# Kernel optimization log

Hardware: AMD Instinct MI355X
Metric: run time of the kernel (lower is better)

The kernel has to match this reference:

```python
import jax, jax.numpy as jnp
import numpy as np

B, NPG, DEG = 256, 128, 16          # graphs per side, nodes per graph, avg degree
N = B * NPG                          # 32768 nodes per side
E = N * DEG                          # 524288 edges per side
F_IN, F1, F2, F3 = 64, 128, 64, 32   # number_labels, filters_1..3
TN, BINS = 16, 16                    # tensor_neurons, bins


def setup_inputs() -> dict:
    key = jax.random.key(0)
    ks = jax.random.split(key, 24)

    def make_edges(k):
        # random edges, each constrained within its own graph block
        base = jax.random.randint(k, (2, E), 0, NPG)
        off = jnp.repeat(jnp.arange(B, dtype=jnp.int64) * NPG, NPG * DEG)
        return (base + off[None, :]).astype(jnp.int64)

    def w(k, shape, fan_in):
        return (jax.random.normal(k, shape, jnp.float32) / np.sqrt(fan_in)).astype(jnp.float32)

    batch = jnp.repeat(jnp.arange(B, dtype=jnp.int64), NPG)
    return {
        'x1': jax.random.normal(ks[0], (N, F_IN), jnp.float32),
        'edge_index_1': make_edges(ks[1]),
        'batch_1': batch,
        'x2': jax.random.normal(ks[2], (N, F_IN), jnp.float32),
        'edge_index_2': make_edges(ks[3]),
        'batch_2': batch,
        # GCN layer params
        'W1': w(ks[4], (F_IN, F1), F_IN), 'b1': jnp.zeros((F1,), jnp.float32),
        'W2': w(ks[5], (F1, F2), F1),     'b2': jnp.zeros((F2,), jnp.float32),
        'W3': w(ks[6], (F2, F3), F2),     'b3': jnp.zeros((F3,), jnp.float32),
        # attention pooling
        'attW': w(ks[7], (F3, F3), F3),
        # tensor network module
        'tW': w(ks[8], (F3, F3, TN), F3),
        'tblock': w(ks[9], (TN, 2 * F3), 2 * F3),
        'tbias': jnp.zeros((TN,), jnp.float32),
        # scoring MLP (feature_count = TN + BINS -> 16 -> 1)
        'sW1': w(ks[10], (TN + BINS, 16), TN + BINS), 'sb1': jnp.zeros((16,), jnp.float32),
        'sW2': w(ks[11], (16, 1), 16),                'sb2': jnp.zeros((1,), jnp.float32),
    }


def _gcn(x, W, b, src, dst):
    # PyG GCNConv: add self-loops, symmetric deg^-1/2 normalization, then scatter-add
    n = x.shape[0]
    loop = jnp.arange(n, dtype=src.dtype)
    s = jnp.concatenate([src, loop])
    d = jnp.concatenate([dst, loop])
    deg = jax.ops.segment_sum(jnp.ones_like(d, dtype=x.dtype), d, num_segments=n)
    dinv = jax.lax.rsqrt(jnp.maximum(deg, 1e-12))
    norm = dinv[s] * dinv[d]                      # [E+N]
    h = x @ W                                     # [N, Fout]
    out = jax.ops.segment_sum(norm[:, None] * h[s], d, num_segments=n)
    return out + b


def _histc(v):
    # torch.histc with bins=BINS, min=max=0 -> uses data min/max; last bin inclusive
    v = v.reshape(-1)
    lo, hi = v.min(), v.max()
    idx = jnp.floor((v - lo) / jnp.maximum(hi - lo, 1e-12) * BINS)
    idx = jnp.clip(idx, 0, BINS - 1).astype(jnp.int32)
    h = jax.ops.segment_sum(jnp.ones_like(v), idx, num_segments=BINS)
    return h / h.sum()


def reference(x1, edge_index_1, batch_1, x2, edge_index_2, batch_2,
              W1, b1, W2, b2, W3, b3, attW, tW, tblock, tbias,
              sW1, sb1, sW2, sb2):
    def conv_pass(x, ei):
        src, dst = ei[0], ei[1]
        h = jax.nn.relu(_gcn(x, W1, b1, src, dst))   # dropout inactive (eval)
        h = jax.nn.relu(_gcn(h, W2, b2, src, dst))
        return _gcn(h, W3, b3, src, dst)

    f1 = conv_pass(x1, edge_index_1)
    f2 = conv_pass(x2, edge_index_2)

    # to_dense_batch: equal-sized, batch-sorted graphs -> plain reshape, full masks
    d1 = f1.reshape(B, NPG, F3)
    d2 = f2.reshape(B, NPG, F3)

    # per-graph-pair similarity histogram (detached in original)
    scores = jnp.einsum('bnd,bmd->bnm', jax.lax.stop_gradient(d1), jax.lax.stop_gradient(d2))
    hist = jax.vmap(_histc)(jax.nn.sigmoid(scores))  # [B, BINS]

    # attention pooling (SimGNN AttentionModule)
    def attn_pool(d):
        ctx = jnp.tanh(jnp.mean(d @ attW, axis=1))             # [B, F3]
        att = jax.nn.sigmoid(jnp.einsum('bnd,bd->bn', d, ctx))  # [B, NPG]
        return jnp.einsum('bnd,bn->bd', d, att)                 # [B, F3]

    e1 = attn_pool(d1)
    e2 = attn_pool(d2)

    # tensor network scoring
    tensor_scores = jnp.einsum('bi,ijk,bj->bk', e1, tW, e2)
    block_scores = jnp.concatenate([e1, e2], axis=-1) @ tblock.T
    tnm = jax.nn.relu(tensor_scores + block_scores + tbias)      # [B, TN]

    feat = jnp.concatenate([tnm, hist], axis=1)                  # [B, TN+BINS]
    h = jax.nn.relu(feat @ sW1 + sb1)
    score = jax.nn.sigmoid(h @ sW2 + sb2)
    return score.squeeze(-1)                                     # [B]
```

## Files before the change

### kernel.cpp

```cpp
#include <hip/hip_runtime.h>
#include <hip/hip_bf16.h>
#include <hip/hip_fp16.h>

#define N_NODES 32768
#define N_EDGES 524288
#define NGRAPH  256
#define NPG     128
#define EPG     2048
#define F_IN    64
#define F1      128
#define F2      64
#define F3      32
#define TN      16
#define BINS    16

typedef _Float16 f16;
typedef _Float16 f16x4 __attribute__((ext_vector_type(4)));
typedef _Float16 f16x8 __attribute__((ext_vector_type(8)));
typedef float    f32x4 __attribute__((ext_vector_type(4)));

__device__ __forceinline__ float sigmoidf(float x) { return 1.f / (1.f + expf(-x)); }

#define L_A    0
#define L_R1   34816
#define L_R2   69632
#define L_R3   88064
#define L_R4   106496
#define L_R5   123904
#define L_DT   128512
#define L_DINV 148992
#define POOLB  149504

#define SA  136
#define SB  72
#define SD  40

template<int N, int K, int AS, int BS, int OS, bool TRANS, bool RELU>
__device__ __forceinline__ void mfma_mm(const f16* __restrict__ A,
                                        const f16* __restrict__ B,
                                        const float* __restrict__ bias,
                                        f16* __restrict__ out, int tid) {
    const int w = tid >> 6, lane = tid & 63;
    const int col = lane & 15, g = lane >> 4;
    const int strip = w & 7, nh = w >> 3;
    const int rowa = strip * 16 + col;
    constexpr int NT = N / 16, KS = K / 32, NT2 = NT / 2;
    f32x4 acc[NT2];
#pragma unroll
    for (int nt = 0; nt < NT2; ++nt) {
        const float b = bias ? bias[(nh * NT2 + nt) * 16 + col] : 0.f;
        acc[nt] = (f32x4){b, b, b, b};
    }
#pragma unroll
    for (int ks = 0; ks < KS; ++ks) {
        const f16x8 a = *(const f16x8*)&A[rowa * AS + ks * 32 + g * 8];
#pragma unroll
        for (int nt = 0; nt < NT2; ++nt) {
            const f16x8 b = *(const f16x8*)&B[((nh * NT2 + nt) * 16 + col) * BS + ks * 32 + g * 8];
            acc[nt] = __builtin_amdgcn_mfma_f32_16x16x32_f16(a, b, acc[nt], 0, 0, 0);
        }
    }
#pragma unroll
    for (int nt = 0; nt < NT2; ++nt) {
        const int c = (nh * NT2 + nt) * 16 + col;
        if (TRANS) {
            f16x4 o;
#pragma unroll
            for (int j = 0; j < 4; ++j) {
                float v = acc[nt][j];
                if (RELU) v = fmaxf(v, 0.f);
                o[j] = (f16)v;
            }
            *(f16x4*)&out[c * OS + strip * 16 + g * 4] = o;
        } else {
#pragma unroll
            for (int j = 0; j < 4; ++j) {
                float v = acc[nt][j];
                if (RELU) v = fmaxf(v, 0.f);
                out[(strip * 16 + g * 4 + j) * OS + c] = (f16)v;
            }
        }
    }
}

__global__ __launch_bounds__(1024, 4) void genn_all(
    const float* __restrict__ x1, const int* __restrict__ ei1,
    const float* __restrict__ x2, const int* __restrict__ ei2,
    const float* __restrict__ W1, const float* __restrict__ b1,
    const float* __restrict__ W2, const float* __restrict__ b2,
    const float* __restrict__ W3, const float* __restrict__ b3,
    const float* __restrict__ attW, const float* __restrict__ tW,
    const float* __restrict__ tblk, const float* __restrict__ tbias,
    const float* __restrict__ sW1, const float* __restrict__ sb1,
    const float* __restrict__ sW2, const float* __restrict__ sb2,
    float* __restrict__ outp) {
    __shared__ __align__(16) char pool[POOLB];
    unsigned int* Acnt = (unsigned int*)(pool + L_A);
    f16*   Amat = (f16*)(pool + L_A);
    f16*   dts  = (f16*)(pool + L_DT);
    float* dinv = (float*)(pool + L_DINV);

    const int g = blockIdx.x;
    const int tid = threadIdx.x;
    const int wv = tid >> 6, lane = tid & 63;

    for (int side = 0; side < 2; ++side) {
        const float* xg = (side ? x2 : x1) + (size_t)g * NPG * F_IN;
        const int* eib  = side ? ei2 : ei1;
        const int* srcg = eib + (size_t)g * EPG;
        const int* dstg = eib + N_EDGES + (size_t)g * EPG;
        const int nb = g * NPG;

        for (int i = tid; i < 2176; i += 1024)
            ((uint4*)Acnt)[i] = make_uint4(0, 0, 0, 0);
        __syncthreads();

#pragma unroll
        for (int it = 0; it < EPG / 1024; ++it) {
            const int e = it * 1024 + tid;
            const int d = dstg[e] - nb;
            const int s = srcg[e] - nb;
            atomicAdd(&Acnt[d * 68 + (s >> 1)], 1u << ((s & 1) << 4));
        }
        {
            f16* xT = (f16*)(pool + L_R1);
#pragma unroll
            for (int it = 0; it < 2; ++it) {
                const int idx = (it * 1024 + tid) * 4;
                const float4 v = *(const float4*)&xg[idx];
                const int n = idx >> 6, c = idx & 63;
                xT[(c + 0) * SA + n] = (f16)v.x;
                xT[(c + 1) * SA + n] = (f16)v.y;
                xT[(c + 2) * SA + n] = (f16)v.z;
                xT[(c + 3) * SA + n] = (f16)v.w;
            }
            f16* W1T = (f16*)(pool + L_R2);
            for (int i = tid; i < F_IN * F1; i += 1024)
                W1T[(i & 127) * SB + (i >> 7)] = (f16)W1[i];
            if (side == 0) {
                f16* W2T = (f16*)(pool + L_R4);
                for (int i = tid; i < F1 * F2; i += 1024)
                    W2T[(i & 63) * SA + (i >> 6)] = (f16)W2[i];
                f16* W3T = (f16*)(pool + L_R5);
                for (int i = tid; i < F2 * F3; i += 1024)
                    W3T[(i & 31) * SB + (i >> 5)] = (f16)W3[i];
            }
        }
        __syncthreads();

        if (tid < 512) {
            const int d = tid >> 2, q = tid & 3;
            unsigned int s = 0;
            const unsigned int* rp = &Acnt[d * 68 + q * 17];
            for (int j = 0; j < 17; ++j) {
                const unsigned int v = rp[j];
                s += (v & 0xffffu) + (v >> 16);
            }
            s += __shfl_down((int)s, 2);
            s += __shfl_down((int)s, 1);
            if (q == 0) dinv[d] = rsqrtf((float)s + 1.0f);
        }
        __syncthreads();

        for (int i = tid; i < 8704; i += 1024) {
            const int d = i / 68, w = i % 68;
            const unsigned int v = Acnt[i];
            const int s0 = 2 * w, s1 = 2 * w + 1;
            int c0 = v & 0xffffu, c1 = v >> 16;
            if (s0 == d) ++c0;
            if (s1 == d) ++c1;
            const float dd = dinv[d];
            const f16 f0 = (f16)((float)c0 * dinv[s0 & 127] * dd);
            const f16 f1 = (f16)((float)c1 * dinv[s1 & 127] * dd);
            unsigned short u0 = __builtin_bit_cast(unsigned short, f0);
            unsigned short u1 = __builtin_bit_cast(unsigned short, f1);
            Acnt[i] = (unsigned int)u0 | ((unsigned int)u1 << 16);
        }
        __syncthreads();

        f16* xT   = (f16*)(pool + L_R1);
        f16* h1   = (f16*)(pool + L_R1);
        f16* W1T  = (f16*)(pool + L_R2);
        f16* h2   = (f16*)(pool + L_R2);
        f16* out1 = (f16*)(pool + L_R3);
        f16* t2T  = (f16*)(pool + L_R3);
        f16* t3T  = (f16*)(pool + L_R3);
        f16* W2T  = (f16*)(pool + L_R4);
        f16* W3T  = (f16*)(pool + L_R5);

        mfma_mm<64, 128, SA, SA, SB, false, false>(Amat, xT, nullptr, out1, tid);
        __syncthreads();
        mfma_mm<128, 64, SB, SB, SA, false, true>(out1, W1T, b1, h1, tid);
        __syncthreads();
        mfma_mm<64, 128, SA, SA, SA, true, false>(h1, W2T, nullptr, t2T, tid);
        __syncthreads();
        mfma_mm<64, 128, SA, SA, SB, false, true>(Amat, t2T, b2, h2, tid);
        __syncthreads();
        mfma_mm<32, 64, SB, SB, SA, true, false>(h2, W3T, nullptr, t3T, tid);
        __syncthreads();
        mfma_mm<32, 128, SA, SA, SD, false, false>(Amat, t3T, b3,
                                                   dts + side * (NPG * SD), tid);
        __syncthreads();
    }

    unsigned char* lhist = (unsigned char*)(pool + L_R4);
    float* pf   = (float*)(pool + L_R3);
    float* red  = pf;
    float* lohi = pf + 32;
    float* meanv= pf + 34;
    float* ctxv = pf + 98;
    float* ev   = pf + 162;
    float* feat = pf + 226;
    float* hv   = pf + 258;
    float* thr  = pf + 274;
    float* av   = pf + 290;
    float* pmean= pf + 546;
    float* ptens= pf + 1570;
    int*   bins2= (int*)(pf + 2082);
    const f16* d1 = dts;
    const f16* d2 = dts + NPG * SD;

    const int col = lane & 15, gq = lane >> 4;
    const int strip = wv & 7, nh = wv >> 3;
    const int rowa = strip * 16 + col;
    f32x4 acc[4];
#pragma unroll
    for (int nt = 0; nt < 4; ++nt) acc[nt] = (f32x4){0.f, 0.f, 0.f, 0.f};
    {
        const f16x8 a = *(const f16x8*)&d1[rowa * SD + gq * 8];
#pragma unroll
        for (int nt = 0; nt < 4; ++nt) {
            const f16x8 b = *(const f16x8*)&d2[((nh * 4 + nt) * 16 + col) * SD + gq * 8];
            acc[nt] = __builtin_amdgcn_mfma_f32_16x16x32_f16(a, b, acc[nt], 0, 0, 0);
        }
    }
    for (int i = tid; i < 4352; i += 1024) ((unsigned int*)lhist)[i] = 0u;
    float lmin = acc[0][0], lmax = acc[0][0];
#pragma unroll
    for (int nt = 0; nt < 4; ++nt)
#pragma unroll
        for (int j = 0; j < 4; ++j) {
            lmin = fminf(lmin, acc[nt][j]);
            lmax = fmaxf(lmax, acc[nt][j]);
        }
    for (int off = 32; off; off >>= 1) {
        lmin = fminf(lmin, __shfl_down(lmin, off));
        lmax = fmaxf(lmax, __shfl_down(lmax, off));
    }
    if (lane == 0) { red[wv] = lmin; red[16 + wv] = lmax; }
    __syncthreads();
    if (tid == 0) {
        float mn = red[0], mx = red[16];
        for (int w = 1; w < 16; ++w) { mn = fminf(mn, red[w]); mx = fmaxf(mx, red[16 + w]); }
        const float los = sigmoidf(mn);
        const float den = fmaxf(sigmoidf(mx) - los, 1e-12f);
        lohi[0] = los;
        lohi[1] = den;
    }
    __syncthreads();
    if (tid < 15) {
        const float p = lohi[0] + (float)(tid + 1) * lohi[1] * (1.f / 16.f);
        thr[tid] = logf(p / (1.f - p));
    }
    __syncthreads();

    {
        unsigned char* lh = &lhist[tid * 17];
#pragma unroll
        for (int nt = 0; nt < 4; ++nt)
#pragma unroll
            for (int j = 0; j < 4; ++j) {
                const float x = acc[nt][j];
                int b = 0;
#pragma unroll
                for (int k = 0; k < 15; ++k) b += (x >= thr[k]) ? 1 : 0;
                lh[b]++;
            }
    }
    __syncthreads();
    if (tid < 256) {
        const int b = tid & 15, chunk = tid >> 4;
        int s = 0;
        for (int i = 0; i < 64; ++i) s += lhist[(chunk * 64 + i) * 17 + b];
        bins2[chunk * 16 + b] = s;
    }
    __syncthreads();

    {
        const int cc = tid & 63, chunk = tid >> 6;
        const int side = cc >> 5, c = cc & 31;
        const f16* dp = dts + side * (NPG * SD);
        float s = 0.f;
        const int nbs = chunk * 8;
        for (int n = 0; n < 8; ++n) s += (float)dp[(nbs + n) * SD + c];
        pmean[chunk * 64 + cc] = s;
    }
    __syncthreads();
    if (tid < 64) {
        float s = 0.f;
        for (int c = 0; c < 16; ++c) s += pmean[c * 64 + tid];
        meanv[tid] = s * (1.f / NPG);
    }
    __syncthreads();
    if (tid < 64) {
        const int c = tid & 31;
        const float* mv = &meanv[(tid >> 5) * 32];
        float a = 0.f;
        for (int k = 0; k < F3; ++k) a += mv[k] * attW[k * F3 + c];
        ctxv[tid] = tanhf(a);
    }
    __syncthreads();
    if (tid < 256) {
        const int n = tid & 127, side = tid >> 7;
        const f16* dp = dts + side * (NPG * SD);
        const float* cx = &ctxv[side * 32];
        float a = 0.f;
        for (int k = 0; k < F3; ++k) a += (float)dp[n * SD + k] * cx[k];
        av[tid] = sigmoidf(a);
    }
    __syncthreads();
    {
        const int cc = tid & 63, chunk = tid >> 6;
        const int side = cc >> 5, c = cc & 31;
        const f16* dp = dts + side * (NPG * SD);
        const float* a = &av[side * 128];
        float s = 0.f;
        const int nbs = chunk * 8;
        for (int n = 0; n < 8; ++n) s += a[nbs + n] * (float)dp[(nbs + n) * SD + c];
        pmean[chunk * 64 + cc] = s;
    }
    __syncthreads();
    if (tid < 64) {
        float s = 0.f;
        for (int c = 0; c < 16; ++c) s += pmean[c * 64 + tid];
        ev[tid] = s;
    }
    __syncthreads();

    if (tid < 512) {
        const int k = tid & 15, i = tid >> 4;
        const float e1i = ev[i];
        float a = 0.f;
        for (int j = 0; j < F3; ++j) a += ev[32 + j] * tW[(i * F3 + j) * TN + k];
        ptens[i * 16 + k] = e1i * a;
    }
    __syncthreads();
    if (tid < TN) {
        float a = tbias[tid];
        for (int i = 0; i < 32; ++i) a += ptens[i * 16 + tid];
        for (int i = 0; i < F3; ++i) a += ev[i] * tblk[tid * 2 * F3 + i];
        for (int j = 0; j < F3; ++j) a += ev[32 + j] * tblk[tid * 2 * F3 + F3 + j];
        feat[tid] = fmaxf(a, 0.f);
    } else if (tid < TN + BINS) {
        const int b = tid - TN;
        int s = 0;
        for (int c = 0; c < 16; ++c) s += bins2[c * 16 + b];
        feat[tid] = (float)s * (1.f / (NPG * NPG));
    }
    __syncthreads();
    if (tid < 16) {
        float a = sb1[tid];
        for (int i = 0; i < TN + BINS; ++i) a += feat[i] * sW1[i * 16 + tid];
        hv[tid] = fmaxf(a, 0.f);
    }
    __syncthreads();
    if (tid == 0) {
        float a = sb2[0];
        for (int j = 0; j < 16; ++j) a += hv[j] * sW2[j];
        outp[g] = sigmoidf(a);
    }
}

extern "C" void kernel_launch(void* const* d_in, const int* in_sizes, int n_in,
                              void* d_out, int out_size, void* d_ws, size_t ws_size,
                              hipStream_t stream) {
    const float* x1   = (const float*)d_in[0];
    const int*   ei1  = (const int*)d_in[1];
    const float* x2   = (const float*)d_in[3];
    const int*   ei2  = (const int*)d_in[4];
    const float* W1   = (const float*)d_in[6];
    const float* b1   = (const float*)d_in[7];
    const float* W2   = (const float*)d_in[8];
    const float* b2   = (const float*)d_in[9];
    const float* W3   = (const float*)d_in[10];
    const float* b3   = (const float*)d_in[11];
    const float* attW = (const float*)d_in[12];
    const float* tW   = (const float*)d_in[13];
    const float* tblk = (const float*)d_in[14];
    const float* tbias= (const float*)d_in[15];
    const float* sW1  = (const float*)d_in[16];
    const float* sb1  = (const float*)d_in[17];
    const float* sW2  = (const float*)d_in[18];
    const float* sb2  = (const float*)d_in[19];
    float* out = (float*)d_out;
    (void)in_sizes; (void)n_in; (void)out_size; (void)d_ws; (void)ws_size;

    genn_all<<<NGRAPH, 1024, 0, stream>>>(x1, ei1, x2, ei2,
                                          W1, b1, W2, b2, W3, b3,
                                          attW, tW, tblk, tbias,
                                          sW1, sb1, sW2, sb2, out);
}
```

Before: 34.87 us.

## Prefetch side-2 inputs, rebalance degree/normalize loops, restructure histogram layout and merge barriers

```diff
diff --git a/kernel.cpp b/kernel.cpp
--- a/kernel.cpp
+++ b/kernel.cpp
@@ -34,6 +34,7 @@
 #define SA  136
 #define SB  72
 #define SD  40
+#define LHS 1040
 
 template<int N, int K, int AS, int BS, int OS, bool TRANS, bool RELU>
 __device__ __forceinline__ void mfma_mm(const f16* __restrict__ A,
@@ -104,11 +105,24 @@
     const int tid = threadIdx.x;
     const int wv = tid >> 6, lane = tid & 63;
 
+    int pre_d[2], pre_s[2];
+    float4 pre_x[2];
+    {
+        const int* s1p = ei2 + (size_t)g * EPG;
+        const int* d1p = ei2 + N_EDGES + (size_t)g * EPG;
+        const float* xg1 = x2 + (size_t)g * NPG * F_IN;
+#pragma unroll
+        for (int it = 0; it < 2; ++it) {
+            pre_d[it] = d1p[it * 1024 + tid];
+            pre_s[it] = s1p[it * 1024 + tid];
+            pre_x[it] = *(const float4*)&xg1[(it * 1024 + tid) * 4];
+        }
+    }
+
     for (int side = 0; side < 2; ++side) {
         const float* xg = (side ? x2 : x1) + (size_t)g * NPG * F_IN;
-        const int* eib  = side ? ei2 : ei1;
-        const int* srcg = eib + (size_t)g * EPG;
-        const int* dstg = eib + N_EDGES + (size_t)g * EPG;
+        const int* srcg = ei1 + (size_t)g * EPG;
+        const int* dstg = ei1 + N_EDGES + (size_t)g * EPG;
         const int nb = g * NPG;
 
         for (int i = tid; i < 2176; i += 1024)
@@ -117,9 +131,9 @@
 
 #pragma unroll
         for (int it = 0; it < EPG / 1024; ++it) {
-            const int e = it * 1024 + tid;
-            const int d = dstg[e] - nb;
-            const int s = srcg[e] - nb;
+            int d, s;
+            if (side == 0) { d = dstg[it * 1024 + tid] - nb; s = srcg[it * 1024 + tid] - nb; }
+            else           { d = pre_d[it] - nb;             s = pre_s[it] - nb; }
             atomicAdd(&Acnt[d * 68 + (s >> 1)], 1u << ((s & 1) << 4));
         }
         {
@@ -127,17 +141,19 @@
 #pragma unroll
             for (int it = 0; it < 2; ++it) {
                 const int idx = (it * 1024 + tid) * 4;
-                const float4 v = *(const float4*)&xg[idx];
+                float4 v;
+                if (side == 0) v = *(const float4*)&xg[idx];
+                else           v = pre_x[it];
                 const int n = idx >> 6, c = idx & 63;
                 xT[(c + 0) * SA + n] = (f16)v.x;
                 xT[(c + 1) * SA + n] = (f16)v.y;
                 xT[(c + 2) * SA + n] = (f16)v.z;
                 xT[(c + 3) * SA + n] = (f16)v.w;
             }
-            f16* W1T = (f16*)(pool + L_R2);
-            for (int i = tid; i < F_IN * F1; i += 1024)
-                W1T[(i & 127) * SB + (i >> 7)] = (f16)W1[i];
             if (side == 0) {
+                f16* W1T = (f16*)(pool + L_R2);
+                for (int i = tid; i < F_IN * F1; i += 1024)
+                    W1T[(i & 127) * SB + (i >> 7)] = (f16)W1[i];
                 f16* W2T = (f16*)(pool + L_R4);
                 for (int i = tid; i < F1 * F2; i += 1024)
                     W2T[(i & 63) * SA + (i >> 6)] = (f16)W2[i];
@@ -148,40 +164,50 @@
         }
         __syncthreads();
 
-        if (tid < 512) {
-            const int d = tid >> 2, q = tid & 3;
+        {
+            const int d = tid >> 3, q = tid & 7;
             unsigned int s = 0;
-            const unsigned int* rp = &Acnt[d * 68 + q * 17];
-            for (int j = 0; j < 17; ++j) {
-                const unsigned int v = rp[j];
-                s += (v & 0xffffu) + (v >> 16);
-            }
+#pragma unroll
+            for (int k = 0; k < 9; ++k) {
+                const int w = q + k * 8;
+                if (w < 68) {
+                    const unsigned int v = Acnt[d * 68 + w];
+                    s += (v & 0xffffu) + (v >> 16);
+                }
+            }
+            s += __shfl_down((int)s, 4);
             s += __shfl_down((int)s, 2);
             s += __shfl_down((int)s, 1);
             if (q == 0) dinv[d] = rsqrtf((float)s + 1.0f);
         }
         __syncthreads();
 
-        for (int i = tid; i < 8704; i += 1024) {
-            const int d = i / 68, w = i % 68;
-            const unsigned int v = Acnt[i];
-            const int s0 = 2 * w, s1 = 2 * w + 1;
-            int c0 = v & 0xffffu, c1 = v >> 16;
-            if (s0 == d) ++c0;
-            if (s1 == d) ++c1;
+        {
+            const int d = tid >> 3, q = tid & 7;
             const float dd = dinv[d];
-            const f16 f0 = (f16)((float)c0 * dinv[s0 & 127] * dd);
-            const f16 f1 = (f16)((float)c1 * dinv[s1 & 127] * dd);
-            unsigned short u0 = __builtin_bit_cast(unsigned short, f0);
-            unsigned short u1 = __builtin_bit_cast(unsigned short, f1);
-            Acnt[i] = (unsigned int)u0 | ((unsigned int)u1 << 16);
+#pragma unroll
+            for (int k = 0; k < 9; ++k) {
+                const int w = q + k * 8;
+                if (w < 68) {
+                    const unsigned int v = Acnt[d * 68 + w];
+                    const int s0 = 2 * w, s1 = 2 * w + 1;
+                    int c0 = v & 0xffffu, c1 = v >> 16;
+                    if (s0 == d) ++c0;
+                    if (s1 == d) ++c1;
+                    const f16 f0 = (f16)((float)c0 * dinv[s0 & 127] * dd);
+                    const f16 f1 = (f16)((float)c1 * dinv[s1 & 127] * dd);
+                    const unsigned short u0 = __builtin_bit_cast(unsigned short, f0);
+                    const unsigned short u1 = __builtin_bit_cast(unsigned short, f1);
+                    Acnt[d * 68 + w] = (unsigned int)u0 | ((unsigned int)u1 << 16);
+                }
+            }
         }
         __syncthreads();
 
         f16* xT   = (f16*)(pool + L_R1);
         f16* h1   = (f16*)(pool + L_R1);
+        f16* h2   = (f16*)(pool + L_R1);
         f16* W1T  = (f16*)(pool + L_R2);
-        f16* h2   = (f16*)(pool + L_R2);
         f16* out1 = (f16*)(pool + L_R3);
         f16* t2T  = (f16*)(pool + L_R3);
         f16* t3T  = (f16*)(pool + L_R3);
@@ -206,17 +232,16 @@
     unsigned char* lhist = (unsigned char*)(pool + L_R4);
     float* pf   = (float*)(pool + L_R3);
     float* red  = pf;
-    float* lohi = pf + 32;
-    float* meanv= pf + 34;
-    float* ctxv = pf + 98;
-    float* ev   = pf + 162;
-    float* feat = pf + 226;
-    float* hv   = pf + 258;
-    float* thr  = pf + 274;
-    float* av   = pf + 290;
-    float* pmean= pf + 546;
-    float* ptens= pf + 1570;
-    int*   bins2= (int*)(pf + 2082);
+    float* meanv= pf + 32;
+    float* ctxv = pf + 96;
+    float* ev   = pf + 160;
+    float* feat = pf + 224;
+    float* hv   = pf + 256;
+    float* thr  = pf + 272;
+    float* av   = pf + 288;
+    float* pmean= pf + 544;
+    float* ptens= pf + 1568;
+    int*   bins2= (int*)(pf + 2080);
     const f16* d1 = dts;
     const f16* d2 = dts + NPG * SD;
 
@@ -234,7 +259,7 @@
             acc[nt] = __builtin_amdgcn_mfma_f32_16x16x32_f16(a, b, acc[nt], 0, 0, 0);
         }
     }
-    for (int i = tid; i < 4352; i += 1024) ((unsigned int*)lhist)[i] = 0u;
+    for (int i = tid; i < 17 * LHS / 4; i += 1024) ((unsigned int*)lhist)[i] = 0u;
     float lmin = acc[0][0], lmax = acc[0][0];
 #pragma unroll
     for (int nt = 0; nt < 4; ++nt)
@@ -249,23 +274,20 @@
     }
     if (lane == 0) { red[wv] = lmin; red[16 + wv] = lmax; }
     __syncthreads();
-    if (tid == 0) {
+    if (tid < 15) {
         float mn = red[0], mx = red[16];
         for (int w = 1; w < 16; ++w) { mn = fminf(mn, red[w]); mx = fmaxf(mx, red[16 + w]); }
-        const float los = sigmoidf(mn);
-        const float den = fmaxf(sigmoidf(mx) - los, 1e-12f);
-        lohi[0] = los;
-        lohi[1] = den;
-    }
-    __syncthreads();
-    if (tid < 15) {
-        const float p = lohi[0] + (float)(tid + 1) * lohi[1] * (1.f / 16.f);
+        const float lo = sigmoidf(mn);
+        const float den = fmaxf(sigmoidf(mx) - lo, 1e-12f);
+        const float p = lo + (float)(tid + 1) * den * (1.f / 16.f);
         thr[tid] = logf(p / (1.f - p));
     }
     __syncthreads();
 
     {
-        unsigned char* lh = &lhist[tid * 17];
+        float tr[15];
+#pragma unroll
+        for (int k = 0; k < 15; ++k) tr[k] = thr[k];
 #pragma unroll
         for (int nt = 0; nt < 4; ++nt)
 #pragma unroll
@@ -273,15 +295,24 @@
                 const float x = acc[nt][j];
                 int b = 0;
 #pragma unroll
-                for (int k = 0; k < 15; ++k) b += (x >= thr[k]) ? 1 : 0;
-                lh[b]++;
+                for (int k = 0; k < 15; ++k) b += (x >= tr[k]) ? 1 : 0;
+                lhist[b * LHS + tid]++;
             }
     }
     __syncthreads();
     if (tid < 256) {
         const int b = tid & 15, chunk = tid >> 4;
+        const unsigned char* row = lhist + b * LHS + chunk * 64;
         int s = 0;
-        for (int i = 0; i < 64; ++i) s += lhist[(chunk * 64 + i) * 17 + b];
+#pragma unroll
+        for (int i = 0; i < 4; ++i) {
+            const uint4 v = *(const uint4*)(row + i * 16);
+            unsigned int u;
+            u = v.x; s += (u & 255) + ((u >> 8) & 255) + ((u >> 16) & 255) + (u >> 24);
+            u = v.y; s += (u & 255) + ((u >> 8) & 255) + ((u >> 16) & 255) + (u >> 24);
+            u = v.z; s += (u & 255) + ((u >> 8) & 255) + ((u >> 16) & 255) + (u >> 24);
+            u = v.w; s += (u & 255) + ((u >> 8) & 255) + ((u >> 16) & 255) + (u >> 24);
+        }
         bins2[chunk * 16 + b] = s;
     }
     __syncthreads();
@@ -296,18 +327,15 @@
         pmean[chunk * 64 + cc] = s;
     }
     __syncthreads();
-    if (tid < 64) {
+    if (wv == 0) {
         float s = 0.f;
-        for (int c = 0; c < 16; ++c) s += pmean[c * 64 + tid];
-        meanv[tid] = s * (1.f / NPG);
-    }
-    __syncthreads();
-    if (tid < 64) {
-        const int c = tid & 31;
-        const float* mv = &meanv[(tid >> 5) * 32];
+        for (int c = 0; c < 16; ++c) s += pmean[c * 64 + lane];
+        meanv[lane] = s * (1.f / NPG);
+        const int c = lane & 31;
+        const float* mv = &meanv[(lane >> 5) * 32];
         float a = 0.f;
         for (int k = 0; k < F3; ++k) a += mv[k] * attW[k * F3 + c];
-        ctxv[tid] = tanhf(a);
+        ctxv[lane] = tanhf(a);
     }
     __syncthreads();
     if (tid < 256) {
```

Result: slower. 49.89 us (+43.1%).
